# Kernel optimization log

Hardware: AMD Instinct MI355X
Metric: run time of the kernel (lower is better)

## Reference

```python
import jax, jax.numpy as jnp
import numpy as np

NEG_INF = -1e30
EPS = 1e-6


def _apply_rope_interleaved(x, cos, sin):
    # x: (..., rope_dim); cos/sin broadcastable to (..., rope_dim//2)
    x1 = x[..., 0::2]
    x2 = x[..., 1::2]
    o1 = x1 * cos - x2 * sin
    o2 = x1 * sin + x2 * cos
    return jnp.stack([o1, o2], axis=-1).reshape(x.shape)


def setup_inputs() -> dict:
    key = jax.random.key(0)
    ks = jax.random.split(key, 6)
    B, S, D = 1, 2048, 7168
    H, HD, ROPE, QLR = 64, 128, 64, 1536
    x = jax.random.normal(ks[0], (B, S, D), dtype=jnp.float32)
    q_lora = jax.random.normal(ks[1], (B, S, QLR), dtype=jnp.float32)
    wq_b = jax.random.normal(ks[2], (QLR, H * HD), dtype=jnp.float32) * 0.02
    wk = jax.random.normal(ks[3], (D, HD), dtype=jnp.float32) * 0.02
    weights_proj = jax.random.normal(ks[4], (D, H), dtype=jnp.float32) * 0.02
    k_norm_w = jnp.ones((HD,), dtype=jnp.float32)
    k_norm_b = jnp.zeros((HD,), dtype=jnp.float32)
    # standard RoPE tables for the first ROPE dims
    half = ROPE // 2
    inv_freq = 1.0 / (10000.0 ** (np.arange(half, dtype=np.float64) / half))
    ang = np.arange(S, dtype=np.float64)[:, None] * inv_freq[None, :]
    cos = jnp.asarray(np.cos(ang), dtype=jnp.float32)
    sin = jnp.asarray(np.sin(ang), dtype=jnp.float32)
    return {"x": x, "q_lora": q_lora, "wq_b": wq_b, "wk": wk,
            "weights_proj": weights_proj, "k_norm_w": k_norm_w,
            "k_norm_b": k_norm_b, "cos": cos, "sin": sin, "topk": 512}


def reference(x, q_lora, wq_b, wk, weights_proj, k_norm_w, k_norm_b, cos, sin, topk):
    B, S, D = x.shape
    HD = wk.shape[1]
    H = weights_proj.shape[1]
    ROPE = cos.shape[1] * 2
    # queries: low-rank up-projection -> per-head, RoPE on first ROPE dims
    q = (q_lora @ wq_b).reshape(B, S, H, HD)
    q_pe = _apply_rope_interleaved(q[..., :ROPE], cos[None, :, None, :], sin[None, :, None, :])
    q = jnp.concatenate([q_pe, q[..., ROPE:]], axis=-1)
    # keys: single head, LayerNorm then RoPE on first ROPE dims
    k = x @ wk  # [B,S,HD]
    mu = k.mean(-1, keepdims=True)
    var = ((k - mu) ** 2).mean(-1, keepdims=True)
    k = (k - mu) * jax.lax.rsqrt(var + EPS) * k_norm_w + k_norm_b
    k_pe = _apply_rope_interleaved(k[..., :ROPE], cos[None], sin[None])
    k = jnp.concatenate([k_pe, k[..., ROPE:]], axis=-1)
    # per-token head gates, scaled by n_heads^-0.5 and softmax scale HD^-0.5
    w = (x @ weights_proj) * (H ** -0.5) * (HD ** -0.5)  # [B,S,H]
    # lightning index score: I[t,s] = sum_h w[t,h] * relu(q[t,h] . k[s])
    scores = jax.nn.relu(jnp.einsum('bshd,btd->bsht', q, k))  # [B,S,H,S]
    index_score = jnp.einsum('bsht,bsh->bst', scores, w)      # [B,S,S]
    # causal mask then top-k token selection
    causal = jnp.arange(S)[None, :] <= jnp.arange(S)[:, None]
    index_score = jnp.where(causal[None], index_score, NEG_INF)
    vals, idx = jax.lax.top_k(index_score, topk)
    return vals, idx
```

## Files before the change

### kernel.cpp

```cpp
#include <hip/hip_runtime.h>
#include <stdint.h>

#define S_LEN 2048
#define D_DIM 7168
#define H_NUM 64
#define HD_DIM 128
#define QLR_DIM 1536
#define NQ_DIM 8192
#define ROPE_DIM 64
#define HALF_DIM 32
#define TOPK_N 512
#define NEG_INF_F (-1e30f)
#define LN_EPS 1e-6f
#define W_SCALE 0.011048543456039806f

#define KCHUNKS 7
#define KCHUNK_SZ 1024
#define NKT 24

#define QF_HSTRIDE (128 * 4 * 64 * 8)

#define QBF_OFF 0
#define ALORA_OFF (QBF_OFF + S_LEN * NQ_DIM / 2)
#define WT_OFF   (ALORA_OFF + S_LEN * QLR_DIM / 2)
#define XBF_OFF  (WT_OFF + NQ_DIM * QLR_DIM / 2)
#define WT2_OFF  (XBF_OFF + S_LEN * D_DIM / 2)
#define KF_OFF   (WT2_OFF + 192 * D_DIM / 2)
#define KBF_OFF  (KF_OFF + S_LEN * HD_DIM)
#define WF_OFF   (KBF_OFF + S_LEN * HD_DIM / 2)
#define SC_OFF   (WF_OFF + S_LEN * H_NUM)

typedef __attribute__((ext_vector_type(8))) short short8;
typedef __attribute__((ext_vector_type(4))) float floatx4;

__device__ __forceinline__ ushort f2bf(float f) {
    unsigned int u = __float_as_uint(f);
    u += 0x7FFFu + ((u >> 16) & 1u);
    return (ushort)(u >> 16);
}
__device__ __forceinline__ unsigned int pack2bf(float lo, float hi) {
    return (unsigned int)f2bf(lo) | ((unsigned int)f2bf(hi) << 16);
}

__device__ __forceinline__ void gld_lds16(const ushort* g, ushort* l) {
    __builtin_amdgcn_global_load_lds(
        (const __attribute__((address_space(1))) unsigned int*)g,
        (__attribute__((address_space(3))) unsigned int*)l, 16, 0, 0);
}

__global__ __launch_bounds__(256) void cast2_bf16_kernel(
    const float* __restrict__ in1, ushort* __restrict__ out1, int nblk1,
    const float* __restrict__ in2, ushort* __restrict__ out2)
{
    int b = blockIdx.x;
    const float* in; ushort* out; int lb;
    if (b < nblk1) { in = in1; out = out1; lb = b; }
    else           { in = in2; out = out2; lb = b - nblk1; }
    int g = (lb * 256 + threadIdx.x) * 8;
    float4 a = *(const float4*)&in[g];
    float4 c = *(const float4*)&in[g + 4];
    uint4 v;
    v.x = pack2bf(a.x, a.y); v.y = pack2bf(a.z, a.w);
    v.z = pack2bf(c.x, c.y); v.w = pack2bf(c.z, c.w);
    *(uint4*)&out[g] = v;
}

__global__ __launch_bounds__(256) void transpose_fused_kernel(
    const float* __restrict__ W, ushort* __restrict__ WT,
    const float* __restrict__ WK, const float* __restrict__ WP,
    ushort* __restrict__ WT2)
{
    __shared__ ushort tl[64][72];
    const int bid = blockIdx.x;
    const int t = threadIdx.x;
    const int r = t >> 4, c4 = (t & 15) * 4;

    if (bid < 3072) {
        const int n0 = (bid & 127) * 64, k0 = (bid >> 7) * 64;
#pragma unroll
        for (int u = 0; u < 4; u++) {
            int kk = r + u * 16;
            float4 v = *(const float4*)&W[(size_t)(k0 + kk) * NQ_DIM + n0 + c4];
            tl[c4 + 0][kk] = f2bf(v.x);
            tl[c4 + 1][kk] = f2bf(v.y);
            tl[c4 + 2][kk] = f2bf(v.z);
            tl[c4 + 3][kk] = f2bf(v.w);
        }
        __syncthreads();
#pragma unroll
        for (int u = 0; u < 2; u++) {
            int i = t + u * 256;
            int nr = i >> 3, c8 = (i & 7) * 8;
            uint4 v = *(const uint4*)&tl[nr][c8];
            *(uint4*)&WT[(size_t)(n0 + nr) * QLR_DIM + k0 + c8] = v;
        }
    } else {
        const int rem = bid - 3072;
        const int ntile = rem % 3;
        const int k0 = (rem / 3) * 64;
        const float* src; int ld, cbase;
        if (ntile < 2) { src = WK; ld = HD_DIM; cbase = ntile * 64; }
        else           { src = WP; ld = H_NUM; cbase = 0; }
#pragma unroll
        for (int u = 0; u < 4; u++) {
            int kk = r + u * 16;
            float4 v = *(const float4*)&src[(size_t)(k0 + kk) * ld + cbase + c4];
            tl[c4 + 0][kk] = f2bf(v.x);
            tl[c4 + 1][kk] = f2bf(v.y);
            tl[c4 + 2][kk] = f2bf(v.z);
            tl[c4 + 3][kk] = f2bf(v.w);
        }
        __syncthreads();
#pragma unroll
        for (int u = 0; u < 2; u++) {
            int i = t + u * 256;
            int nr = i >> 3, c8 = (i & 7) * 8;
            uint4 v = *(const uint4*)&tl[nr][c8];
            *(uint4*)&WT2[(size_t)(ntile * 64 + nr) * D_DIM + k0 + c8] = v;
        }
    }
}

__global__ __launch_bounds__(512, 2) void qgemm_mfma_kernel(
    const ushort* __restrict__ Abf,
    const ushort* __restrict__ WT,
    const float* __restrict__ cosp, const float* __restrict__ sinp,
    ushort* __restrict__ Qo)
{
    __shared__ __align__(16) ushort lds[65536];

    const int tid = threadIdx.x;
    const int lane = tid & 63;
    const int wave = tid >> 6;
    const int m = lane & 15;
    const int q = lane >> 4;
    const int wm = wave & 1;
    const int wn = wave >> 1;

    const int wg = blockIdx.x;
    const int xcd = wg & 7, lid = wg >> 3;
    const int bx = xcd * 4 + (lid & 3);
    const int by = lid >> 2;
    const int m0 = by * 256;
    const int n0 = bx * 256;

    const ushort* sgA[2][2];
    const ushort* sgB[2][2];
    unsigned int ldoff[2][2];
#pragma unroll
    for (int h = 0; h < 2; h++)
#pragma unroll
        for (int r = 0; r < 2; r++) {
            int s = r * 512 + wave * 64 + lane;
            int row = s >> 3, c = s & 7;
            int kg = c ^ (row & 7);
            sgA[h][r] = Abf + (size_t)(m0 + h * 128 + row) * QLR_DIM + kg * 8;
            sgB[h][r] = WT  + (size_t)(n0 + h * 128 + row) * QLR_DIM + kg * 8;
            ldoff[h][r] = (unsigned int)(h * 8192 + (r * 512 + wave * 64) * 8);
        }

    auto stageA = [&](int kt, int h) {
        ushort* dbase = &lds[(kt & 1) * 16384];
        gld_lds16(sgA[h][0] + kt * 64, dbase + ldoff[h][0]);
        gld_lds16(sgA[h][1] + kt * 64, dbase + ldoff[h][1]);
    };
    auto stageB = [&](int kt, int h) {
        ushort* dbase = &lds[32768 + (kt & 1) * 16384];
        gld_lds16(sgB[h][0] + kt * 64, dbase + ldoff[h][0]);
        gld_lds16(sgB[h][1] + kt * 64, dbase + ldoff[h][1]);
    };

    unsigned int aoff[2], boff[2];
#pragma unroll
    for (int ks = 0; ks < 2; ks++) {
        unsigned int xr = (unsigned int)(((((ks << 2) + q) ^ (m & 7))) * 8);
        aoff[ks] = (unsigned int)((wm * 128 + m) * 64) + xr;
        boff[ks] = (unsigned int)((wn * 64 + m) * 64) + xr;
    }

    floatx4 acc[8][4];
#pragma unroll
    for (int i = 0; i < 8; i++)
#pragma unroll
        for (int j = 0; j < 4; j++) acc[i][j] = (floatx4){0.f, 0.f, 0.f, 0.f};

    stageA(0, 0); stageA(0, 1); stageB(0, 0); stageB(0, 1);
    asm volatile("s_waitcnt vmcnt(0)" ::: "memory");
    __builtin_amdgcn_s_barrier();

#pragma unroll 2
    for (int kt = 0; kt < NKT; ++kt) {
        const ushort* as = &lds[(kt & 1) * 16384];
        const ushort* bs = &lds[32768 + (kt & 1) * 16384];
        const bool pf = (kt + 1 < NKT);

        short8 af[4], bf0[4], bf1[4];

#pragma unroll
        for (int mt = 0; mt < 4; mt++)
            af[mt] = *(const short8*)&as[aoff[0] + mt * 1024];
#pragma unroll
        for (int nt = 0; nt < 4; nt++)
            bf0[nt] = *(const short8*)&bs[boff[0] + nt * 1024];
        if (pf) { stageA(kt + 1, 0); stageA(kt + 1, 1); stageB(kt + 1, 0); }
        __builtin_amdgcn_s_barrier();
        __builtin_amdgcn_s_setprio(1);
#pragma unroll
        for (int mt = 0; mt < 4; mt++)
#pragma unroll
            for (int nt = 0; nt < 4; nt++)
                acc[mt][nt] = __builtin_amdgcn_mfma_f32_16x16x32_bf16(
                    af[mt], bf0[nt], acc[mt][nt], 0, 0, 0);
        __builtin_amdgcn_s_setprio(0);
        __builtin_amdgcn_s_barrier();

#pragma unroll
        for (int mt = 0; mt < 4; mt++)
            af[mt] = *(const short8*)&as[aoff[1] + mt * 1024];
#pragma unroll
        for (int nt = 0; nt < 4; nt++)
            bf1[nt] = *(const short8*)&bs[boff[1] + nt * 1024];
        if (pf) stageB(kt + 1, 1);
        __builtin_amdgcn_s_barrier();
        __builtin_amdgcn_s_setprio(1);
#pragma unroll
        for (int mt = 0; mt < 4; mt++)
#pragma unroll
            for (int nt = 0; nt < 4; nt++)
                acc[mt][nt] = __builtin_amdgcn_mfma_f32_16x16x32_bf16(
                    af[mt], bf1[nt], acc[mt][nt], 0, 0, 0);
        __builtin_amdgcn_s_setprio(0);
        __builtin_amdgcn_s_barrier();

#pragma unroll
        for (int mt = 0; mt < 4; mt++)
            af[mt] = *(const short8*)&as[aoff[0] + 4096 + mt * 1024];
        __builtin_amdgcn_s_barrier();
        __builtin_amdgcn_s_setprio(1);
#pragma unroll
        for (int mt = 0; mt < 4; mt++)
#pragma unroll
            for (int nt = 0; nt < 4; nt++)
                acc[4 + mt][nt] = __builtin_amdgcn_mfma_f32_16x16x32_bf16(
                    af[mt], bf0[nt], acc[4 + mt][nt], 0, 0, 0);
        __builtin_amdgcn_s_setprio(0);
        __builtin_amdgcn_s_barrier();

#pragma unroll
        for (int mt = 0; mt < 4; mt++)
            af[mt] = *(const short8*)&as[aoff[1] + 4096 + mt * 1024];
        __builtin_amdgcn_s_barrier();
        __builtin_amdgcn_s_setprio(1);
#pragma unroll
        for (int mt = 0; mt < 4; mt++)
#pragma unroll
            for (int nt = 0; nt < 4; nt++)
                acc[4 + mt][nt] = __builtin_amdgcn_mfma_f32_16x16x32_bf16(
                    af[mt], bf1[nt], acc[4 + mt][nt], 0, 0, 0);
        __builtin_amdgcn_s_setprio(0);
        asm volatile("s_waitcnt vmcnt(0)" ::: "memory");
        __builtin_amdgcn_s_barrier();
    }

    __syncthreads();
    ushort* ep = lds;
    const int h0 = bx * 2;
    const int sgrp0 = m0 >> 4;

#pragma unroll
    for (int hh = 0; hh < 2; hh++) {
        if ((wn >> 1) == hh) {
            const int dbase = (wn & 1) * 64;
            const bool do_rope = ((wn & 1) == 0);
#pragma unroll
            for (int ai = 0; ai < 8; ai++) {
                const int srow0 = m0 + wm * 128 + (ai & 3) * 16 + (ai >> 2) * 64 + q * 4;
                const int lrow0 = srow0 - m0;
#pragma unroll
                for (int bj = 0; bj < 4; bj++) {
                    const int d = dbase + bj * 16 + m;
                    float o[4];
                    if (do_rope) {
                        const int jj = d >> 1;
#pragma unroll
                        for (int r = 0; r < 4; r++) {
                            float x = acc[(ai >> 2) * 4 + (ai & 3)][bj][r];
                            float p = __shfl_xor(x, 1, 64);
                            float c = cosp[(srow0 + r) * HALF_DIM + jj];
                            float sn = sinp[(srow0 + r) * HALF_DIM + jj];
                            o[r] = (d & 1) ? (p * sn + x * c) : (x * c - p * sn);
                        }
                    } else {
#pragma unroll
                        for (int r = 0; r < 4; r++)
                            o[r] = acc[(ai >> 2) * 4 + (ai & 3)][bj][r];
                    }
#pragma unroll
                    for (int r = 0; r < 4; r++)
                        ep[(lrow0 + r) * 136 + d] = f2bf(o[r]);
                }
            }
        }
        __syncthreads();
        const size_t hstr = (size_t)(h0 + hh) * QF_HSTRIDE;
#pragma unroll
        for (int u = 0; u < 8; u++) {
            int i = u * 512 + tid;
            int sgl = i >> 8, c = i & 255;
            int ks = c >> 6, ln = c & 63;
            int srow = sgl * 16 + (ln & 15);
            int d0 = (ks << 5) + ((ln >> 4) << 3);
            uint4 v = *(const uint4*)&ep[srow * 136 + d0];
            *(uint4*)&Qo[hstr + ((((size_t)(sgrp0 + sgl) * 4 + ks) * 64 + ln) * 8)] = v;
        }
        __syncthreads();
    }
}

__global__ __launch_bounds__(256) void kw_mfma_kernel(
    const ushort* __restrict__ Xbf,
    const ushort* __restrict__ WT2,
    float* __restrict__ partial)
{
    __shared__ ushort As[128 * 64];
    __shared__ ushort Bs[64 * 64];

    const int tid = threadIdx.x;
    const int lane = tid & 63;
    const int wave = tid >> 6;
    const int m = lane & 15;
    const int q = lane >> 4;
    const int wm = wave & 1, wn = wave >> 1;
    const int m0 = blockIdx.x * 128;
    const int n0 = blockIdx.y * 64;
    const int kc = blockIdx.z;
    const size_t kbase = (size_t)kc * KCHUNK_SZ;

    const ushort* agp[4];
    unsigned int abase[4];
#pragma unroll
    for (int u = 0; u < 4; u++) {
        int s = (u * 4 + wave) * 64 + lane;
        int row = s >> 3, c = s & 7;
        int kg = c ^ (row & 7);
        agp[u] = Xbf + (size_t)(m0 + row) * D_DIM + kbase + kg * 8;
        abase[u] = (unsigned int)((u * 4 + wave) * 64 * 8);
    }
    const ushort* bgp[2];
    unsigned int bbase[2];
#pragma unroll
    for (int u = 0; u < 2; u++) {
        int s = (u * 4 + wave) * 64 + lane;
        int row = s >> 3, c = s & 7;
        int kg = c ^ (row & 7);
        bgp[u] = WT2 + (size_t)(n0 + row) * D_DIM + kbase + kg * 8;
        bbase[u] = (unsigned int)((u * 4 + wave) * 64 * 8);
    }

    floatx4 acc[4][2];
#pragma unroll
    for (int i = 0; i < 4; i++)
#pragma unroll
        for (int j = 0; j < 2; j++) acc[i][j] = (floatx4){0.f, 0.f, 0.f, 0.f};

    for (int kt = 0; kt < KCHUNK_SZ; kt += 64) {
        __syncthreads();
#pragma unroll
        for (int u = 0; u < 4; u++) gld_lds16(agp[u] + kt, &As[abase[u]]);
#pragma unroll
        for (int u = 0; u < 2; u++) gld_lds16(bgp[u] + kt, &Bs[bbase[u]]);
        __syncthreads();

        short8 af[4][2], bfr[2][2];
#pragma unroll
        for (int mt = 0; mt < 4; mt++) {
            int row = wm * 64 + mt * 16 + m;
#pragma unroll
            for (int ks = 0; ks < 2; ks++)
                af[mt][ks] = *(const short8*)
                    &As[row * 64 + ((((ks << 2) + q) ^ (m & 7)) * 8)];
        }
#pragma unroll
        for (int nt = 0; nt < 2; nt++) {
            int row = wn * 32 + nt * 16 + m;
#pragma unroll
            for (int ks = 0; ks < 2; ks++)
                bfr[nt][ks] = *(const short8*)
                    &Bs[row * 64 + ((((ks << 2) + q) ^ (m & 7)) * 8)];
        }
#pragma unroll
        for (int mt = 0; mt < 4; mt++)
#pragma unroll
            for (int nt = 0; nt < 2; nt++)
#pragma unroll
                for (int ks = 0; ks < 2; ks++)
                    acc[mt][nt] = __builtin_amdgcn_mfma_f32_16x16x32_bf16(
                        af[mt][ks], bfr[nt][ks], acc[mt][nt], 0, 0, 0);
    }

#pragma unroll
    for (int mt = 0; mt < 4; mt++) {
        int grow = m0 + wm * 64 + mt * 16 + q * 4;
#pragma unroll
        for (int nt = 0; nt < 2; nt++) {
            int gn = n0 + wn * 32 + nt * 16 + m;
#pragma unroll
            for (int r = 0; r < 4; r++)
                partial[((size_t)kc * S_LEN + grow + r) * 192 + gn] = acc[mt][nt][r];
        }
    }
}

__global__ __launch_bounds__(192) void kw_reduce_norm_kernel(
    const float* __restrict__ partial,
    const float* __restrict__ gw, const float* __restrict__ gb,
    const float* __restrict__ cosp, const float* __restrict__ sinp,
    ushort* __restrict__ Kbf, float* __restrict__ Wo)
{
    __shared__ float red[128];
    __shared__ float sh[128];
    const int m = blockIdx.x, t = threadIdx.x;

    float s = 0.f;
#pragma unroll
    for (int c = 0; c < KCHUNKS; c++)
        s += partial[((size_t)c * S_LEN + m) * 192 + t];

    if (t >= HD_DIM)
        Wo[(size_t)m * H_NUM + (t - HD_DIM)] = s * W_SCALE;

    if (t < HD_DIM) red[t] = s;
    __syncthreads();
    for (int off = 64; off > 0; off >>= 1) {
        if (t < off) red[t] += red[t + off];
        __syncthreads();
    }
    float mu = red[0] * (1.f / HD_DIM);
    __syncthreads();
    float dv = s - mu;
    if (t < HD_DIM) red[t] = dv * dv;
    __syncthreads();
    for (int off = 64; off > 0; off >>= 1) {
        if (t < off) red[t] += red[t + off];
        __syncthreads();
    }
    float var = red[0] * (1.f / HD_DIM);
    float rs = rsqrtf(var + LN_EPS);
    float kn = 0.f;
    if (t < HD_DIM) { kn = dv * rs * gw[t] + gb[t]; sh[t] = kn; }
    __syncthreads();
    if (t < HD_DIM) {
        float out;
        if (t < ROPE_DIM) {
            int jj = t >> 1;
            float c = cosp[m * HALF_DIM + jj], sn = sinp[m * HALF_DIM + jj];
            out = ((t & 1) == 0) ? (sh[t] * c - sh[t + 1] * sn)
                                 : (sh[t - 1] * sn + sh[t] * c);
        } else {
            out = kn;
        }
        Kbf[(size_t)m * HD_DIM + t] = f2bf(out);
    }
}

__global__ __launch_bounds__(256, 2) void attn_mfma_kernel(
    const ushort* __restrict__ Qb,
    const ushort* __restrict__ Kb,
    const float* __restrict__ Wf,
    float* __restrict__ SC)
{
    __shared__ float Wsm[64 * 68];

    const int bidx = blockIdx.x;
    const int x = bidx & 7, j = bidx >> 3;
    const int g1 = x + 1, g2 = 32 - x, g3 = x + 9;
    int ts, tt;
    if (j < g1)                { ts = x;      tt = j; }
    else if (j < g1 + g2)      { ts = 31 - x; tt = j - g1; }
    else if (j < g1 + g2 + g3) { ts = x + 8;  tt = j - g1 - g2; }
    else                       { ts = 23 - x; tt = j - g1 - g2 - g3; }
    const int s0 = ts * 64, t0 = tt * 64;

    const int tid = threadIdx.x;
    const int lane = tid & 63;
    const int m = lane & 15;
    const int q = lane >> 4;
    const int strip = (tid >> 6) * 16;

    {
        const float4* gw = (const float4*)(Wf + (size_t)s0 * H_NUM);
#pragma unroll
        for (int u = 0; u < 4; u++) {
            int ch = tid + u * 256;
            float4 v = gw[ch];
            *(float4*)&Wsm[(ch >> 4) * 68 + (ch & 15) * 4] = v;
        }
    }

    short8 bf[4][4];
#pragma unroll
    for (int tile = 0; tile < 4; tile++)
#pragma unroll
        for (int ks = 0; ks < 4; ks++)
            bf[tile][ks] = *(const short8*)
                &Kb[(size_t)(t0 + tile * 16 + m) * HD_DIM + ks * 32 + q * 8];

    __syncthreads();

    float acc[4][4];
#pragma unroll
    for (int tile = 0; tile < 4; tile++)
#pragma unroll
        for (int r = 0; r < 4; r++) acc[tile][r] = 0.f;

    const int sgrp = ts * 4 + (strip >> 4);
    const ushort* qfb = Qb + ((size_t)sgrp * 4 * 64 + lane) * 8;
    const float* wrow = &Wsm[(strip + q * 4) * 68];

    auto loadQ = [&](short8* dst, int h) {
        const ushort* p = qfb + (size_t)h * QF_HSTRIDE;
#pragma unroll
        for (int ks = 0; ks < 4; ks++) dst[ks] = *(const short8*)&p[ks * 512];
    };
    auto computeH = [&](const short8* af, int h) {
        float wv[4];
#pragma unroll
        for (int r = 0; r < 4; r++) wv[r] = wrow[r * 68 + h];
#pragma unroll
        for (int tile = 0; tile < 4; tile++) {
            floatx4 p = {0.f, 0.f, 0.f, 0.f};
#pragma unroll
            for (int ks = 0; ks < 4; ks++)
                p = __builtin_amdgcn_mfma_f32_16x16x32_bf16(af[ks], bf[tile][ks], p, 0, 0, 0);
#pragma unroll
            for (int r = 0; r < 4; r++)
                acc[tile][r] += fmaxf(p[r], 0.f) * wv[r];
        }
    };

    short8 afA[4], afB[4];
    loadQ(afA, 0);
    for (int h = 0; h < H_NUM; h += 2) {
        loadQ(afB, h + 1);
        computeH(afA, h);
        if (h + 2 < H_NUM) loadQ(afA, h + 2);
        computeH(afB, h + 1);
    }

#pragma unroll
    for (int tile = 0; tile < 4; tile++)
#pragma unroll
        for (int r = 0; r < 4; r++)
            SC[(size_t)(s0 + strip + q * 4 + r) * S_LEN + t0 + tile * 16 + m] =
                acc[tile][r];
}

__device__ __forceinline__ unsigned int fkey(float f) {
    unsigned int u = __float_as_uint(f);
    return (u & 0x80000000u) ? ~u : (u | 0x80000000u);
}

__global__ __launch_bounds__(256) void topk_kernel(
    const float* __restrict__ SC, float* __restrict__ outv, float* __restrict__ outi)
{
    __shared__ unsigned int key[S_LEN];
    __shared__ float val[S_LEN];
    const int s = blockIdx.x, tid = threadIdx.x;
    const int nchunks = (s >> 9) + 1;
    const int nact = nchunks << 9;

    for (int t = tid; t < nact; t += 256) {
        float v = (t <= s) ? SC[(size_t)s * S_LEN + t] : NEG_INF_F;
        val[t] = v;
        key[t] = (fkey(v) & 0xFFFFF800u) | (unsigned int)(S_LEN - 1 - t);
    }
    __syncthreads();

    for (int k2 = 2; k2 <= 512; k2 <<= 1) {
        for (int j = k2 >> 1; j > 0; j >>= 1) {
            for (int p = tid; p < (nact >> 1); p += 256) {
                int i = 2 * p - (p & (j - 1));
                int il = i & 511;
                unsigned int a = key[i], b = key[i + j];
                bool up = ((il & k2) == 0);
                bool sw = up ? (a < b) : (a > b);
                if (sw) { key[i] = b; key[i + j] = a; }
            }
            __syncthreads();
        }
    }

    for (int c = 1; c < nchunks; c++) {
        for (int p = tid; p < 512; p += 256) {
            unsigned int a = key[p], b = key[(c << 9) + 511 - p];
            key[p] = a > b ? a : b;
        }
        __syncthreads();
        for (int j = 256; j > 0; j >>= 1) {
            int p = tid;
            int i = 2 * p - (p & (j - 1));
            unsigned int a = key[i], b = key[i + j];
            if (a < b) { key[i] = b; key[i + j] = a; }
            __syncthreads();
        }
    }

    for (int i2 = tid; i2 < TOPK_N; i2 += 256) {
        unsigned int kv = key[i2];
        int t = S_LEN - 1 - (int)(kv & 0x7FFu);
        outv[(size_t)s * TOPK_N + i2] = val[t];
        outi[(size_t)s * TOPK_N + i2] = (float)t;
    }
}

extern "C" void kernel_launch(void* const* d_in, const int* in_sizes, int n_in,
                              void* d_out, int out_size, void* d_ws, size_t ws_size,
                              hipStream_t stream)
{
    (void)in_sizes; (void)n_in; (void)out_size; (void)ws_size;
    const float* x      = (const float*)d_in[0];
    const float* q_lora = (const float*)d_in[1];
    const float* wq_b   = (const float*)d_in[2];
    const float* wk     = (const float*)d_in[3];
    const float* wproj  = (const float*)d_in[4];
    const float* knw    = (const float*)d_in[5];
    const float* knb    = (const float*)d_in[6];
    const float* cosp   = (const float*)d_in[7];
    const float* sinp   = (const float*)d_in[8];

    float* ws = (float*)d_ws;
    ushort* Qbf  = (ushort*)(ws + QBF_OFF);
    ushort* Albf = (ushort*)(ws + ALORA_OFF);
    ushort* WTbf = (ushort*)(ws + WT_OFF);
    ushort* Xbf  = (ushort*)(ws + XBF_OFF);
    ushort* WT2  = (ushort*)(ws + WT2_OFF);
    ushort* Kbf  = (ushort*)(ws + KBF_OFF);
    float*  Wf   = ws + WF_OFF;
    float*  SCb  = ws + SC_OFF;
    float*  partial = ws + SC_OFF;

    float* outv = (float*)d_out;
    float* outi = outv + (size_t)S_LEN * TOPK_N;

    const int nblk_qlora = (S_LEN * QLR_DIM) / (256 * 8);
    const int nblk_x     = (S_LEN * D_DIM) / (256 * 8);

    cast2_bf16_kernel<<<nblk_qlora + nblk_x, 256, 0, stream>>>(
        q_lora, Albf, nblk_qlora, x, Xbf);
    transpose_fused_kernel<<<3072 + 336, 256, 0, stream>>>(
        wq_b, WTbf, wk, wproj, WT2);
    kw_mfma_kernel<<<dim3(S_LEN / 128, 3, KCHUNKS), 256, 0, stream>>>(Xbf, WT2, partial);
    kw_reduce_norm_kernel<<<S_LEN, 192, 0, stream>>>(
        partial, knw, knb, cosp, sinp, Kbf, Wf);
    qgemm_mfma_kernel<<<256, 512, 0, stream>>>(Albf, WTbf, cosp, sinp, Qbf);
    attn_mfma_kernel<<<528, 256, 0, stream>>>(Qbf, Kbf, Wf, SCb);
    topk_kernel<<<S_LEN, 256, 0, stream>>>(SCb, outv, outi);
}
```

Measured before the change: 329.4 us.

## Merge prep kernels, double-buffer kw GEMM, add MFMA priority, widen topk blocks

Merges the bf16 cast and weight-transpose kernels into one prep launch, removing one launch and its inter-kernel gap. The kw GEMM now double-buffers LDS and issues the next tile's loads before the MFMAs, with s_setprio around the MFMA blocks so loads and compute overlap. The attention kernel also raises priority around its MFMAs. The top-k sort runs with 512 threads per block, which halves the loop iterations per thread but raises register and occupancy pressure.

```diff
diff --git a/kernel.cpp b/kernel.cpp
--- a/kernel.cpp
+++ b/kernel.cpp
@@ -30,6 +30,13 @@
 #define WF_OFF   (KBF_OFF + S_LEN * HD_DIM / 2)
 #define SC_OFF   (WF_OFF + S_LEN * H_NUM)
 
+#define PREP_CAST_QL 1536
+#define PREP_CAST_X  7168
+#define PREP_CAST_BLKS (PREP_CAST_QL + PREP_CAST_X)
+#define PREP_WQB_BLKS 3072
+#define PREP_WKP_BLKS 336
+#define PREP_TOTAL (PREP_CAST_BLKS + PREP_WQB_BLKS + PREP_WKP_BLKS)
+
 typedef __attribute__((ext_vector_type(8))) short short8;
 typedef __attribute__((ext_vector_type(4))) float floatx4;
 
@@ -48,34 +55,35 @@
         (__attribute__((address_space(3))) unsigned int*)l, 16, 0, 0);
 }
 
-__global__ __launch_bounds__(256) void cast2_bf16_kernel(
-    const float* __restrict__ in1, ushort* __restrict__ out1, int nblk1,
-    const float* __restrict__ in2, ushort* __restrict__ out2)
-{
-    int b = blockIdx.x;
-    const float* in; ushort* out; int lb;
-    if (b < nblk1) { in = in1; out = out1; lb = b; }
-    else           { in = in2; out = out2; lb = b - nblk1; }
-    int g = (lb * 256 + threadIdx.x) * 8;
-    float4 a = *(const float4*)&in[g];
-    float4 c = *(const float4*)&in[g + 4];
-    uint4 v;
-    v.x = pack2bf(a.x, a.y); v.y = pack2bf(a.z, a.w);
-    v.z = pack2bf(c.x, c.y); v.w = pack2bf(c.z, c.w);
-    *(uint4*)&out[g] = v;
-}
-
-__global__ __launch_bounds__(256) void transpose_fused_kernel(
+__global__ __launch_bounds__(256) void prep_kernel(
+    const float* __restrict__ q_lora, ushort* __restrict__ Albf,
+    const float* __restrict__ x, ushort* __restrict__ Xbf,
     const float* __restrict__ W, ushort* __restrict__ WT,
     const float* __restrict__ WK, const float* __restrict__ WP,
     ushort* __restrict__ WT2)
 {
     __shared__ ushort tl[64][72];
-    const int bid = blockIdx.x;
+    const int b = blockIdx.x;
     const int t = threadIdx.x;
+
+    if (b < PREP_CAST_BLKS) {
+        const float* in; ushort* out; int lb;
+        if (b < PREP_CAST_QL) { in = q_lora; out = Albf; lb = b; }
+        else                  { in = x;      out = Xbf;  lb = b - PREP_CAST_QL; }
+        int g = (lb * 256 + t) * 8;
+        float4 a = *(const float4*)&in[g];
+        float4 c = *(const float4*)&in[g + 4];
+        uint4 v;
+        v.x = pack2bf(a.x, a.y); v.y = pack2bf(a.z, a.w);
+        v.z = pack2bf(c.x, c.y); v.w = pack2bf(c.z, c.w);
+        *(uint4*)&out[g] = v;
+        return;
+    }
+
+    const int bid = b - PREP_CAST_BLKS;
     const int r = t >> 4, c4 = (t & 15) * 4;
 
-    if (bid < 3072) {
+    if (bid < PREP_WQB_BLKS) {
         const int n0 = (bid & 127) * 64, k0 = (bid >> 7) * 64;
 #pragma unroll
         for (int u = 0; u < 4; u++) {
@@ -95,7 +103,7 @@
             *(uint4*)&WT[(size_t)(n0 + nr) * QLR_DIM + k0 + c8] = v;
         }
     } else {
-        const int rem = bid - 3072;
+        const int rem = bid - PREP_WQB_BLKS;
         const int ntile = rem % 3;
         const int k0 = (rem / 3) * 64;
         const float* src; int ld, cbase;
@@ -322,8 +330,8 @@
     const ushort* __restrict__ WT2,
     float* __restrict__ partial)
 {
-    __shared__ ushort As[128 * 64];
-    __shared__ ushort Bs[64 * 64];
+    __shared__ ushort As[2 * 128 * 64];
+    __shared__ ushort Bs[2 * 64 * 64];
 
     const int tid = threadIdx.x;
     const int lane = tid & 63;
@@ -357,45 +365,73 @@
         bbase[u] = (unsigned int)((u * 4 + wave) * 64 * 8);
     }
 
+    auto stage = [&](int t) {
+        ushort* da = &As[(t & 1) * 8192];
+        ushort* db = &Bs[(t & 1) * 4096];
+#pragma unroll
+        for (int u = 0; u < 4; u++) gld_lds16(agp[u] + t * 64, da + abase[u]);
+#pragma unroll
+        for (int u = 0; u < 2; u++) gld_lds16(bgp[u] + t * 64, db + bbase[u]);
+    };
+
     floatx4 acc[4][2];
 #pragma unroll
     for (int i = 0; i < 4; i++)
 #pragma unroll
         for (int j = 0; j < 2; j++) acc[i][j] = (floatx4){0.f, 0.f, 0.f, 0.f};
 
-    for (int kt = 0; kt < KCHUNK_SZ; kt += 64) {
-        __syncthreads();
-#pragma unroll
-        for (int u = 0; u < 4; u++) gld_lds16(agp[u] + kt, &As[abase[u]]);
-#pragma unroll
-        for (int u = 0; u < 2; u++) gld_lds16(bgp[u] + kt, &Bs[bbase[u]]);
-        __syncthreads();
-
-        short8 af[4][2], bfr[2][2];
+    stage(0);
+    __syncthreads();
+
+#pragma unroll 2
+    for (int t = 0; t < KCHUNK_SZ / 64; ++t) {
+        const ushort* as = &As[(t & 1) * 8192];
+        const ushort* bs = &Bs[(t & 1) * 4096];
+
+        short8 af[4], bfr[2];
+
 #pragma unroll
         for (int mt = 0; mt < 4; mt++) {
             int row = wm * 64 + mt * 16 + m;
-#pragma unroll
-            for (int ks = 0; ks < 2; ks++)
-                af[mt][ks] = *(const short8*)
-                    &As[row * 64 + ((((ks << 2) + q) ^ (m & 7)) * 8)];
+            af[mt] = *(const short8*)&as[row * 64 + ((q ^ (m & 7)) * 8)];
         }
 #pragma unroll
         for (int nt = 0; nt < 2; nt++) {
             int row = wn * 32 + nt * 16 + m;
-#pragma unroll
-            for (int ks = 0; ks < 2; ks++)
-                bfr[nt][ks] = *(const short8*)
-                    &Bs[row * 64 + ((((ks << 2) + q) ^ (m & 7)) * 8)];
-        }
+            bfr[nt] = *(const short8*)&bs[row * 64 + ((q ^ (m & 7)) * 8)];
+        }
+        if (t + 1 < KCHUNK_SZ / 64) stage(t + 1);
+        __builtin_amdgcn_s_barrier();
+        __builtin_amdgcn_s_setprio(1);
 #pragma unroll
         for (int mt = 0; mt < 4; mt++)
 #pragma unroll
             for (int nt = 0; nt < 2; nt++)
-#pragma unroll
-                for (int ks = 0; ks < 2; ks++)
-                    acc[mt][nt] = __builtin_amdgcn_mfma_f32_16x16x32_bf16(
-                        af[mt][ks], bfr[nt][ks], acc[mt][nt], 0, 0, 0);
+                acc[mt][nt] = __builtin_amdgcn_mfma_f32_16x16x32_bf16(
+                    af[mt], bfr[nt], acc[mt][nt], 0, 0, 0);
+        __builtin_amdgcn_s_setprio(0);
+        __builtin_amdgcn_s_barrier();
+
+#pragma unroll
+        for (int mt = 0; mt < 4; mt++) {
+            int row = wm * 64 + mt * 16 + m;
+            af[mt] = *(const short8*)&as[row * 64 + (((4 + q) ^ (m & 7)) * 8)];
+        }
+#pragma unroll
+        for (int nt = 0; nt < 2; nt++) {
+            int row = wn * 32 + nt * 16 + m;
+            bfr[nt] = *(const short8*)&bs[row * 64 + (((4 + q) ^ (m & 7)) * 8)];
+        }
+        __builtin_amdgcn_s_barrier();
+        __builtin_amdgcn_s_setprio(1);
+#pragma unroll
+        for (int mt = 0; mt < 4; mt++)
+#pragma unroll
+            for (int nt = 0; nt < 2; nt++)
+                acc[mt][nt] = __builtin_amdgcn_mfma_f32_16x16x32_bf16(
+                    af[mt], bfr[nt], acc[mt][nt], 0, 0, 0);
+        __builtin_amdgcn_s_setprio(0);
+        __syncthreads();
     }
 
 #pragma unroll
@@ -529,9 +565,11 @@
 #pragma unroll
         for (int tile = 0; tile < 4; tile++) {
             floatx4 p = {0.f, 0.f, 0.f, 0.f};
+            __builtin_amdgcn_s_setprio(1);
 #pragma unroll
             for (int ks = 0; ks < 4; ks++)
                 p = __builtin_amdgcn_mfma_f32_16x16x32_bf16(af[ks], bf[tile][ks], p, 0, 0, 0);
+            __builtin_amdgcn_s_setprio(0);
 #pragma unroll
             for (int r = 0; r < 4; r++)
                 acc[tile][r] += fmaxf(p[r], 0.f) * wv[r];
@@ -560,7 +598,7 @@
     return (u & 0x80000000u) ? ~u : (u | 0x80000000u);
 }
 
-__global__ __launch_bounds__(256) void topk_kernel(
+__global__ __launch_bounds__(512) void topk_kernel(
     const float* __restrict__ SC, float* __restrict__ outv, float* __restrict__ outi)
 {
     __shared__ unsigned int key[S_LEN];
@@ -569,7 +607,7 @@
     const int nchunks = (s >> 9) + 1;
     const int nact = nchunks << 9;
 
-    for (int t = tid; t < nact; t += 256) {
+    for (int t = tid; t < nact; t += 512) {
         float v = (t <= s) ? SC[(size_t)s * S_LEN + t] : NEG_INF_F;
         val[t] = v;
         key[t] = (fkey(v) & 0xFFFFF800u) | (unsigned int)(S_LEN - 1 - t);
@@ -578,7 +616,7 @@
 
     for (int k2 = 2; k2 <= 512; k2 <<= 1) {
         for (int j = k2 >> 1; j > 0; j >>= 1) {
-            for (int p = tid; p < (nact >> 1); p += 256) {
+            for (int p = tid; p < (nact >> 1); p += 512) {
                 int i = 2 * p - (p & (j - 1));
                 int il = i & 511;
                 unsigned int a = key[i], b = key[i + j];
@@ -591,21 +629,23 @@
     }
 
     for (int c = 1; c < nchunks; c++) {
-        for (int p = tid; p < 512; p += 256) {
+        {
+            int p = tid;
             unsigned int a = key[p], b = key[(c << 9) + 511 - p];
             key[p] = a > b ? a : b;
         }
         __syncthreads();
         for (int j = 256; j > 0; j >>= 1) {
-            int p = tid;
-            int i = 2 * p - (p & (j - 1));
-            unsigned int a = key[i], b = key[i + j];
-            if (a < b) { key[i] = b; key[i + j] = a; }
+            if (tid < 256) {
+                int i = 2 * tid - (tid & (j - 1));
+                unsigned int a = key[i], b = key[i + j];
+                if (a < b) { key[i] = b; key[i + j] = a; }
+            }
             __syncthreads();
         }
     }
 
-    for (int i2 = tid; i2 < TOPK_N; i2 += 256) {
+    for (int i2 = tid; i2 < TOPK_N; i2 += 512) {
         unsigned int kv = key[i2];
         int t = S_LEN - 1 - (int)(kv & 0x7FFu);
         outv[(size_t)s * TOPK_N + i2] = val[t];
@@ -642,17 +682,12 @@
     float* outv = (float*)d_out;
     float* outi = outv + (size_t)S_LEN * TOPK_N;
 
-    const int nblk_qlora = (S_LEN * QLR_DIM) / (256 * 8);
-    const int nblk_x     = (S_LEN * D_DIM) / (256 * 8);
-
-    cast2_bf16_kernel<<<nblk_qlora + nblk_x, 256, 0, stream>>>(
-        q_lora, Albf, nblk_qlora, x, Xbf);
-    transpose_fused_kernel<<<3072 + 336, 256, 0, stream>>>(
-        wq_b, WTbf, wk, wproj, WT2);
+    prep_kernel<<<PREP_TOTAL, 256, 0, stream>>>(
+        q_lora, Albf, x, Xbf, wq_b, WTbf, wk, wproj, WT2);
     kw_mfma_kernel<<<dim3(S_LEN / 128, 3, KCHUNKS), 256, 0, stream>>>(Xbf, WT2, partial);
     kw_reduce_norm_kernel<<<S_LEN, 192, 0, stream>>>(
         partial, knw, knb, cosp, sinp, Kbf, Wf);
     qgemm_mfma_kernel<<<256, 512, 0, stream>>>(Albf, WTbf, cosp, sinp, Qbf);
     attn_mfma_kernel<<<528, 256, 0, stream>>>(Qbf, Kbf, Wf, SCb);
-    topk_kernel<<<S_LEN, 256, 0, stream>>>(SCb, outv, outi);
-}
+    topk_kernel<<<S_LEN, 512, 0, stream>>>(SCb, outv, outi);
+}
```

Result: no change. 334.9 us (+1.7%).
